# Optimization experiments

Measured on AMD Instinct MI355X. Metric: run time of the kernel, lower is better.

## Reference

```python
import jax, jax.numpy as jnp
import numpy as np


def _one_sided_chamfer(a, b):
    # a: [B, N, 3], b: [B, M, 3]
    # squared pairwise distances via ||a||^2 + ||b||^2 - 2 a.b
    a2 = jnp.sum(a * a, axis=-1)              # [B, N]
    b2 = jnp.sum(b * b, axis=-1)              # [B, M]
    ab = jnp.einsum('bnd,bmd->bnm', a, b)     # [B, N, M]
    d2 = a2[:, :, None] + b2[:, None, :] - 2.0 * ab
    d2 = jnp.maximum(d2, 0.0)                 # numerical floor
    # nearest neighbor in b for each point of a, averaged
    return jnp.mean(jnp.min(d2, axis=2))


def setup_inputs() -> dict:
    key = jax.random.key(0)
    k1, k2 = jax.random.split(key)
    B, N, D = 8, 8192, 3
    predict_pc = jax.random.normal(k1, (B, N, D), dtype=jnp.float32)
    gt_pc = jax.random.normal(k2, (B, N, D), dtype=jnp.float32)
    return {"predict_pc": predict_pc, "gt_pc": gt_pc}


def reference(predict_pc, gt_pc):
    dist1 = _one_sided_chamfer(predict_pc, gt_pc)
    dist2 = _one_sided_chamfer(gt_pc, predict_pc)
    return (dist1 + dist2) / 2.0
```

## Files before the change

kernel.cpp:

```cpp
#include <hip/hip_runtime.h>


#define BATCH   8
#define NPTS    8192
#define BLK     256
#define TOTAL_A (2 * BATCH * NPTS)
#define NCH4    4
#define BQUART  (NPTS / NCH4)
#define CHUNK   256
#define NCHUNK  (BQUART / CHUNK)
#define TPC     (CHUNK / 32)
#define ABLKS   (NPTS / 256)
#define P1_BLOCKS (2 * BATCH * ABLKS * NCH4)
#define P2_BLOCKS (TOTAL_A / BLK)
#define SC      16.0f

typedef _Float16 f16x8  __attribute__((ext_vector_type(8)));
typedef float    f32x16 __attribute__((ext_vector_type(16)));
typedef __attribute__((address_space(1))) const void gptr_t;
typedef __attribute__((address_space(3))) void lptr_t;

static __device__ __forceinline__ unsigned int pk2(float a, float b) {
  unsigned short ua = __builtin_bit_cast(unsigned short, (_Float16)a);
  unsigned short ub = __builtin_bit_cast(unsigned short, (_Float16)b);
  return (unsigned int)ua | ((unsigned int)ub << 16);
}

static __device__ __forceinline__ float fold16(float mq, f32x16 d) {
  float t0 = fmaxf(fmaxf(d[0],  d[1]),  d[2]);
  float t1 = fmaxf(fmaxf(d[3],  d[4]),  d[5]);
  float t2 = fmaxf(fmaxf(d[6],  d[7]),  d[8]);
  float t3 = fmaxf(fmaxf(d[9],  d[10]), d[11]);
  float t4 = fmaxf(fmaxf(d[12], d[13]), d[14]);
  float t5 = fmaxf(fmaxf(t0, t1), t2);
  float t6 = fmaxf(fmaxf(t3, t4), d[15]);
  return fmaxf(fmaxf(mq, t5), t6);
}

static __device__ __forceinline__ void fmt_point(float X, float Y, float Z,
                                                 uint4* lo, uint4* hi) {
  float x = X * SC, y = Y * SC, z = Z * SC;
  float fx = (float)(_Float16)x, fy = (float)(_Float16)y, fz = (float)(_Float16)z;
  float lx = x - fx, ly = y - fy, lz = z - fz;
  float b2 = fmaf(x, x, fmaf(y, y, z * z));
  float c  = -0.5f * b2;
  float fc = (float)(_Float16)c;
  float lc = c - fc;
  *lo = make_uint4(pk2(x, y), pk2(z, lx), pk2(ly, lz), pk2(x, y));
  *hi = make_uint4(pk2(z, c), pk2(lc, 1.0f), 0x00003C00u, 0u);
}

static __device__ __forceinline__ f16x8 make_afrag(float X, float Y, float Z,
                                                   int hi) {
  float x = X * SC, y = Y * SC, z = Z * SC;
  float fx = (float)(_Float16)x, fy = (float)(_Float16)y, fz = (float)(_Float16)z;
  float lx = x - fx, ly = y - fy, lz = z - fz;
  float a2 = fmaf(x, x, fmaf(y, y, z * z));
  float dd = -0.5f * a2;
  float fd = (float)(_Float16)dd;
  float ld = dd - fd;
  uint4 u;
  if (!hi) {
    u = make_uint4(pk2(x, y), pk2(z, x), pk2(y, z), pk2(lx, ly));
  } else {
    u = make_uint4(pk2(lz, 1.0f), pk2(1.0f, dd), pk2(ld, 0.0f), 0u);
  }
  return __builtin_bit_cast(f16x8, u);
}

__global__ __launch_bounds__(BLK) void chamfer_fmt(
    const float* __restrict__ pred, const float* __restrict__ gt,
    uint4* __restrict__ fmt, unsigned int* __restrict__ counter) {
  const int gid = blockIdx.x * BLK + threadIdx.x;
  if (gid == 0) *counter = 0u;
  const int arr = gid >> 16;
  const int idx = gid & 65535;
  const float* src = arr ? gt : pred;
  float X = src[(size_t)idx * 3 + 0];
  float Y = src[(size_t)idx * 3 + 1];
  float Z = src[(size_t)idx * 3 + 2];
  uint4 lo, hi;
  fmt_point(X, Y, Z, &lo, &hi);
  const int region = gid >> 13;
  const int p      = gid & 8191;
  size_t base = (size_t)region * 16384 + (size_t)(p >> 5) * 64 + (p & 31);
  fmt[base]      = lo;
  fmt[base + 32] = hi;
}

static __device__ __forceinline__ void stage_chunk(const uint4* src,
                                                   uint4* dst,
                                                   int wave, int lane) {
#pragma unroll
  for (int k = 0; k < 2; ++k) {
    const uint4* g = src + wave * 128 + k * 64 + lane;
    uint4*       l = dst + wave * 128 + k * 64;
    __builtin_amdgcn_global_load_lds((gptr_t*)g, (lptr_t*)l, 16, 0, 0);
  }
}

__global__ __launch_bounds__(BLK, 8) void chamfer_mfma_pass1(
    const float* __restrict__ pred, const float* __restrict__ gt,
    const uint4* __restrict__ fmt, float* __restrict__ partial) {
  __shared__ uint4 lds4[2 * 512];

  const int swz   = ((blockIdx.x & 7) << 8) | (blockIdx.x >> 3);
  const int qc    = swz & 3;
  const int r     = swz >> 2;
  const int ablk  = r & (ABLKS - 1);
  const int bd    = r >> 5;
  const int batch = bd & 7;
  const int side  = bd >> 3;

  const float* A    = side ? gt : pred;
  const uint4* fmtB = fmt + (size_t)((1 - side) * 8 + batch) * 16384
                          + (size_t)qc * 4096;

  const int t    = threadIdx.x;
  const int lane = t & 63;
  const int wave = t >> 6;
  const int col  = lane & 31;
  const int hi   = lane >> 5;

  const float* Ab = A + ((size_t)batch * NPTS + (size_t)ablk * 256 + (size_t)wave * 64) * 3;
  f16x8 af0 = make_afrag(Ab[col * 3 + 0], Ab[col * 3 + 1], Ab[col * 3 + 2], hi);
  f16x8 af1 = make_afrag(Ab[(32 + col) * 3 + 0], Ab[(32 + col) * 3 + 1],
                         Ab[(32 + col) * 3 + 2], hi);
  float mq0 = -3.0e38f, mq1 = -3.0e38f;
  const f32x16 zero = {};

  stage_chunk(fmtB, lds4, wave, lane);
  __syncthreads();

  for (int c = 0; c < NCHUNK; ++c) {
    const uint4* rbuf = lds4 + (c & 1) * 512;
    if (c + 1 < NCHUNK)
      stage_chunk(fmtB + (size_t)(c + 1) * 512, lds4 + ((c + 1) & 1) * 512,
                  wave, lane);

#pragma unroll
    for (int tt = 0; tt < TPC; ++tt) {
      f16x8 bf = *(const f16x8*)(rbuf + tt * 64 + lane);
      f32x16 d0 = __builtin_amdgcn_mfma_f32_32x32x16_f16(bf, af0, zero, 0, 0, 0);
      f32x16 d1 = __builtin_amdgcn_mfma_f32_32x32x16_f16(bf, af1, zero, 0, 0, 0);
      mq0 = fold16(mq0, d0);
      mq1 = fold16(mq1, d1);
    }
    __syncthreads();
  }

  mq0 = fmaxf(mq0, __shfl_xor(mq0, 32));
  mq1 = fmaxf(mq1, __shfl_xor(mq1, 32));

  if (lane < 32) {
    size_t a0 = (size_t)bd * NPTS + (size_t)ablk * 256 + (size_t)wave * 64 + col;
    partial[a0 * NCH4 + qc]        = mq0;
    partial[(a0 + 32) * NCH4 + qc] = mq1;
  }
}

__global__ __launch_bounds__(BLK) void chamfer_pass2fin(
    const float4* __restrict__ partial, float* __restrict__ blockSums,
    unsigned int* __restrict__ counter, float* __restrict__ out) {
  __shared__ float wsum[BLK / 64];
  __shared__ int amLast;

  const int gid = blockIdx.x * BLK + threadIdx.x;
  float4 p = partial[gid];
  float m  = fmaxf(fmaxf(p.x, p.y), fmaxf(p.z, p.w));
  float d2 = fmaxf(m * (-1.0f / 128.0f), 0.0f);

  const int lane = threadIdx.x & 63, wave = threadIdx.x >> 6;
  float v = d2;
  for (int off = 32; off > 0; off >>= 1) v += __shfl_down(v, off);
  if (lane == 0) wsum[wave] = v;
  __syncthreads();
  if (threadIdx.x == 0) {
    float s = (wsum[0] + wsum[1]) + (wsum[2] + wsum[3]);
    blockSums[blockIdx.x] = s;
    __threadfence();
    unsigned int prev = atomicAdd(counter, 1u);
    amLast = (prev == P2_BLOCKS - 1);
  }
  __syncthreads();

  if (amLast) {
    __threadfence();
    const volatile float* vbs = blockSums;
    float v2 = vbs[threadIdx.x] + vbs[threadIdx.x + 256];
    for (int off = 32; off > 0; off >>= 1) v2 += __shfl_down(v2, off);
    if (lane == 0) wsum[wave] = v2;
    __syncthreads();
    if (threadIdx.x == 0) {
      float s = ((wsum[0] + wsum[1]) + wsum[2]) + wsum[3];
      out[0] = s * (1.0f / (float)TOTAL_A);
    }
  }
}

extern "C" void kernel_launch(void* const* d_in, const int* in_sizes, int n_in,
                              void* d_out, int out_size, void* d_ws, size_t ws_size,
                              hipStream_t stream) {
  const float* pred = (const float*)d_in[0];
  const float* gt   = (const float*)d_in[1];
  float* out = (float*)d_out;

  uint4*        fmtb      = (uint4*)d_ws;
  float*        partial   = (float*)((char*)d_ws + (size_t)TOTAL_A * 32);
  float*        blockSums = partial + (size_t)TOTAL_A * NCH4;
  unsigned int* counter   = (unsigned int*)(blockSums + P2_BLOCKS);

  chamfer_fmt<<<TOTAL_A / BLK, BLK, 0, stream>>>(pred, gt, fmtb, counter);
  chamfer_mfma_pass1<<<P1_BLOCKS, BLK, 0, stream>>>(pred, gt, fmtb, partial);
  chamfer_pass2fin<<<P2_BLOCKS, BLK, 0, stream>>>((const float4*)partial,
                                                  blockSums, counter, out);
}
```

Before: 102.1 us.

## Drop LDS staging, read B fragments from global, double A points per wave

The pass-1 kernel no longer stages B-point chunks into LDS through global_load_lds double buffering. Each lane now loads its B fragment straight from global memory (L1/L2 cached). Each wave now holds four A fragments (128 points) instead of two, so every loaded B fragment feeds four MFMAs. That halves the grid and cuts B traffic per A point, but it lowers the occupancy hint to 4 and makes load latency depend on cache hits and unrolling rather than explicit prefetch. Periodic s_barrier calls keep the waves roughly in step, presumably so they share cache lines.

```diff
diff --git a/kernel.cpp b/kernel.cpp
--- a/kernel.cpp
+++ b/kernel.cpp
@@ -7,18 +7,15 @@
 #define TOTAL_A (2 * BATCH * NPTS)
 #define NCH4    4
 #define BQUART  (NPTS / NCH4)
-#define CHUNK   256
-#define NCHUNK  (BQUART / CHUNK)
-#define TPC     (CHUNK / 32)
-#define ABLKS   (NPTS / 256)
+#define NTILES  (BQUART / 32)
+#define ABLK_SZ 512
+#define ABLKS   (NPTS / ABLK_SZ)
 #define P1_BLOCKS (2 * BATCH * ABLKS * NCH4)
 #define P2_BLOCKS (TOTAL_A / BLK)
 #define SC      16.0f
 
 typedef _Float16 f16x8  __attribute__((ext_vector_type(8)));
 typedef float    f32x16 __attribute__((ext_vector_type(16)));
-typedef __attribute__((address_space(1))) const void gptr_t;
-typedef __attribute__((address_space(3))) void lptr_t;
 
 static __device__ __forceinline__ unsigned int pk2(float a, float b) {
   unsigned short ua = __builtin_bit_cast(unsigned short, (_Float16)a);
@@ -88,27 +85,14 @@
   fmt[base + 32] = hi;
 }
 
-static __device__ __forceinline__ void stage_chunk(const uint4* src,
-                                                   uint4* dst,
-                                                   int wave, int lane) {
-#pragma unroll
-  for (int k = 0; k < 2; ++k) {
-    const uint4* g = src + wave * 128 + k * 64 + lane;
-    uint4*       l = dst + wave * 128 + k * 64;
-    __builtin_amdgcn_global_load_lds((gptr_t*)g, (lptr_t*)l, 16, 0, 0);
-  }
-}
-
-__global__ __launch_bounds__(BLK, 8) void chamfer_mfma_pass1(
+__global__ __launch_bounds__(BLK, 4) void chamfer_mfma_pass1(
     const float* __restrict__ pred, const float* __restrict__ gt,
     const uint4* __restrict__ fmt, float* __restrict__ partial) {
-  __shared__ uint4 lds4[2 * 512];
-
-  const int swz   = ((blockIdx.x & 7) << 8) | (blockIdx.x >> 3);
+  const int swz   = ((blockIdx.x & 7) << 7) | (blockIdx.x >> 3);
   const int qc    = swz & 3;
   const int r     = swz >> 2;
   const int ablk  = r & (ABLKS - 1);
-  const int bd    = r >> 5;
+  const int bd    = r >> 4;
   const int batch = bd & 7;
   const int side  = bd >> 3;
 
@@ -122,40 +106,49 @@
   const int col  = lane & 31;
   const int hi   = lane >> 5;
 
-  const float* Ab = A + ((size_t)batch * NPTS + (size_t)ablk * 256 + (size_t)wave * 64) * 3;
-  f16x8 af0 = make_afrag(Ab[col * 3 + 0], Ab[col * 3 + 1], Ab[col * 3 + 2], hi);
-  f16x8 af1 = make_afrag(Ab[(32 + col) * 3 + 0], Ab[(32 + col) * 3 + 1],
-                         Ab[(32 + col) * 3 + 2], hi);
-  float mq0 = -3.0e38f, mq1 = -3.0e38f;
+  const float* Ab = A + ((size_t)batch * NPTS + (size_t)ablk * ABLK_SZ
+                         + (size_t)wave * 128) * 3;
+  f16x8 af0 = make_afrag(Ab[(0 * 32 + col) * 3 + 0], Ab[(0 * 32 + col) * 3 + 1],
+                         Ab[(0 * 32 + col) * 3 + 2], hi);
+  f16x8 af1 = make_afrag(Ab[(1 * 32 + col) * 3 + 0], Ab[(1 * 32 + col) * 3 + 1],
+                         Ab[(1 * 32 + col) * 3 + 2], hi);
+  f16x8 af2 = make_afrag(Ab[(2 * 32 + col) * 3 + 0], Ab[(2 * 32 + col) * 3 + 1],
+                         Ab[(2 * 32 + col) * 3 + 2], hi);
+  f16x8 af3 = make_afrag(Ab[(3 * 32 + col) * 3 + 0], Ab[(3 * 32 + col) * 3 + 1],
+                         Ab[(3 * 32 + col) * 3 + 2], hi);
+  float mq0 = -3.0e38f, mq1 = -3.0e38f, mq2 = -3.0e38f, mq3 = -3.0e38f;
   const f32x16 zero = {};
 
-  stage_chunk(fmtB, lds4, wave, lane);
-  __syncthreads();
-
-  for (int c = 0; c < NCHUNK; ++c) {
-    const uint4* rbuf = lds4 + (c & 1) * 512;
-    if (c + 1 < NCHUNK)
-      stage_chunk(fmtB + (size_t)(c + 1) * 512, lds4 + ((c + 1) & 1) * 512,
-                  wave, lane);
-
-#pragma unroll
-    for (int tt = 0; tt < TPC; ++tt) {
-      f16x8 bf = *(const f16x8*)(rbuf + tt * 64 + lane);
+  const uint4* bp = fmtB + lane;
+
+  for (int g = 0; g < 4; ++g) {
+#pragma unroll 4
+    for (int tt = g * 16; tt < g * 16 + 16; ++tt) {
+      f16x8 bf = *(const f16x8*)(bp + (size_t)tt * 64);
       f32x16 d0 = __builtin_amdgcn_mfma_f32_32x32x16_f16(bf, af0, zero, 0, 0, 0);
+      mq0 = fold16(mq0, d0);
       f32x16 d1 = __builtin_amdgcn_mfma_f32_32x32x16_f16(bf, af1, zero, 0, 0, 0);
-      mq0 = fold16(mq0, d0);
       mq1 = fold16(mq1, d1);
+      f32x16 d2 = __builtin_amdgcn_mfma_f32_32x32x16_f16(bf, af2, zero, 0, 0, 0);
+      mq2 = fold16(mq2, d2);
+      f32x16 d3 = __builtin_amdgcn_mfma_f32_32x32x16_f16(bf, af3, zero, 0, 0, 0);
+      mq3 = fold16(mq3, d3);
     }
-    __syncthreads();
+    if (g < 3) __builtin_amdgcn_s_barrier();
   }
 
   mq0 = fmaxf(mq0, __shfl_xor(mq0, 32));
   mq1 = fmaxf(mq1, __shfl_xor(mq1, 32));
+  mq2 = fmaxf(mq2, __shfl_xor(mq2, 32));
+  mq3 = fmaxf(mq3, __shfl_xor(mq3, 32));
 
   if (lane < 32) {
-    size_t a0 = (size_t)bd * NPTS + (size_t)ablk * 256 + (size_t)wave * 64 + col;
-    partial[a0 * NCH4 + qc]        = mq0;
+    size_t a0 = (size_t)bd * NPTS + (size_t)ablk * ABLK_SZ
+              + (size_t)wave * 128 + col;
+    partial[(a0 + 0)  * NCH4 + qc] = mq0;
     partial[(a0 + 32) * NCH4 + qc] = mq1;
+    partial[(a0 + 64) * NCH4 + qc] = mq2;
+    partial[(a0 + 96) * NCH4 + qc] = mq3;
   }
 }
 
```

Result: slower. 184.4 us (+80.5%).
